# Performance work log

Measured on AMD Instinct MI355X. Metric: run time of the kernel, lower is better.

## Reference

```python
import jax, jax.numpy as jnp
import numpy as np
import math

V, E, H, A, N = 32000, 512, 512, 64, 8  # vocab, embed, rnn hidden, att_size, n_heads
T, B = 256, 128                          # scan length (acts as att batch), inner dim


def _lstm(x, Wih, Whh, bih, bhh):
    # x: (T, B, E); torch nn.LSTM gate order i, f, g, o; zero initial state
    Bb = x.shape[1]
    Hh = Whh.shape[1]
    init = (jnp.zeros((Bb, Hh), x.dtype), jnp.zeros((Bb, Hh), x.dtype))

    def step(carry, xt):
        h, c = carry
        gates = xt @ Wih.T + bih + h @ Whh.T + bhh          # (B, 4H)
        i, f, g, o = jnp.split(gates, 4, axis=-1)
        c = jax.nn.sigmoid(f) * c + jax.nn.sigmoid(i) * jnp.tanh(g)
        h = jax.nn.sigmoid(o) * jnp.tanh(c)
        return (h, c), h

    _, hs = jax.lax.scan(step, init, x)
    return hs  # (T, B, H)


def setup_inputs() -> dict:
    key = jax.random.key(0)
    ks = jax.random.split(key, 26)
    rn = lambda k, s: jax.random.normal(k, s, jnp.float32) * 0.02
    inp = {
        "input_seq_l": jax.random.randint(ks[0], (T, B), 0, V, jnp.int32),
        "input_seq_r": jax.random.randint(ks[1], (T, B), 0, V, jnp.int32),
        "emb_l": rn(ks[2], (V, E)),
        "emb_r": rn(ks[3], (V, E)),
        "Wih_l": rn(ks[4], (4 * H, E)), "Whh_l": rn(ks[5], (4 * H, H)),
        "bih_l": rn(ks[6], (4 * H,)), "bhh_l": rn(ks[7], (4 * H,)),
        "Wih_r": rn(ks[8], (4 * H, E)), "Whh_r": rn(ks[9], (4 * H, H)),
        "bih_r": rn(ks[10], (4 * H,)), "bhh_r": rn(ks[11], (4 * H,)),
        "Wq": rn(ks[12], (N, H, A)), "bq": rn(ks[13], (N, A)),
        "Wk": rn(ks[14], (N, H, A)), "bk": rn(ks[15], (N, A)),
        "Wv": rn(ks[16], (N, H, A)), "bv": rn(ks[17], (N, A)),
        "Wo": rn(ks[18], (N * A, H)), "bo": rn(ks[19], (H,)),
        "Wh": rn(ks[20], (2 * H, 64)), "bh": rn(ks[21], (64,)),
        "Wa": rn(ks[22], (64, 2)), "ba": rn(ks[23], (2,)),
    }
    return inp


def reference(input_seq_l, input_seq_r, emb_l, emb_r,
              Wih_l, Whh_l, bih_l, bhh_l,
              Wih_r, Whh_r, bih_r, bhh_r,
              Wq, bq, Wk, bk, Wv, bv, Wo, bo, Wh, bh, Wa, ba):
    # left encoder
    ol = _lstm(emb_l[input_seq_l], Wih_l, Whh_l, bih_l, bhh_l)   # (T, B, H)
    # multi-head attention over left outputs (all heads batched)
    q = jnp.einsum('tbh,nhd->ntbd', ol, Wq) + bq[:, None, None, :]
    k = jnp.einsum('tbh,nhd->ntbd', ol, Wk) + bk[:, None, None, :]
    v = jnp.einsum('tbh,nhd->ntbd', ol, Wv) + bv[:, None, None, :]
    scores = jnp.einsum('ntbd,ntcd->ntbc', q, k) / math.sqrt(A)  # (N, T, B, B)
    p = jax.nn.softmax(scores, axis=-1)
    att = jnp.einsum('ntbc,ntcd->ntbd', p, v)                    # (N, T, B, A)
    att = att.transpose(1, 2, 0, 3).reshape(att.shape[1], att.shape[2], -1)  # (T, B, N*A)
    ol = att @ Wo + bo                                           # (T, B, H)
    ol = ol.mean(axis=1)                                         # (T, H)
    # right encoder
    orr = _lstm(emb_r[input_seq_r], Wih_r, Whh_r, bih_r, bhh_r).mean(axis=1)  # (T, H)
    cat = jnp.concatenate([ol, orr], axis=1)                     # (T, 2H)
    fc = cat @ Wh + bh
    ans = jax.nn.softmax(fc @ Wa + ba, axis=1)                   # (T, 2)
    return ans
```

## Files before the change

kernel.cpp:

```cpp
#include <hip/hip_runtime.h>

typedef unsigned short u16;
typedef __attribute__((ext_vector_type(4))) float f32x4;
typedef __attribute__((ext_vector_type(8))) short bf8;

#define MFMA16(a, b, c) __builtin_amdgcn_mfma_f32_16x16x32_bf16((a), (b), (c), 0, 0, 0)

__device__ __forceinline__ u16 f2bf(float f) {
  unsigned u = __builtin_bit_cast(unsigned, f);
  u += 0x7FFFu + ((u >> 16) & 1u);
  return (u16)(u >> 16);
}
__device__ __forceinline__ float bf2f(u16 h) {
  unsigned u = ((unsigned)h) << 16;
  return __builtin_bit_cast(float, u);
}
__device__ __forceinline__ float sigm(float x) { return 1.0f / (1.0f + __expf(-x)); }
__device__ __forceinline__ float tanh_f(float x) {
  x = fminf(fmaxf(x, -15.f), 15.f);
  float e = __expf(2.f * x);
  return (e - 1.f) / (e + 1.f);
}

__global__ void k_cast(const float* __restrict__ in, u16* __restrict__ out, int n4) {
  int i = blockIdx.x * blockDim.x + threadIdx.x;
  if (i >= n4) return;
  float4 v = ((const float4*)in)[i];
  union { u16 h[4]; uint2 u; } p;
  p.h[0] = f2bf(v.x); p.h[1] = f2bf(v.y); p.h[2] = f2bf(v.z); p.h[3] = f2bf(v.w);
  ((uint2*)out)[i] = p.u;
}

__global__ void k_bsum(const float* __restrict__ a, const float* __restrict__ b,
                       float* __restrict__ o, int n) {
  int i = blockIdx.x * blockDim.x + threadIdx.x;
  if (i < n) o[i] = a[i] + b[i];
}

__global__ void k_zero32(unsigned* __restrict__ p, int n) {
  int i = blockIdx.x * blockDim.x + threadIdx.x;
  if (i < n) p[i] = 0u;
}

__global__ void k_fill(float* __restrict__ p, int n, float v) {
  int i = blockIdx.x * blockDim.x + threadIdx.x;
  if (i < n) p[i] = v;
}

__global__ void k_tqkv(const float* __restrict__ W, u16* __restrict__ WT) {
  int g = blockIdx.x * blockDim.x + threadIdx.x;
  int n = g >> 15, d = (g >> 9) & 63, h = g & 511;
  WT[g] = f2bf(W[(n << 15) + (h << 6) + d]);
}

__device__ __forceinline__ void gemm_body(
    const int* __restrict__ idx, const float* __restrict__ emb,
    const float* __restrict__ Wih, u16* __restrict__ Gpre,
    int m_base, int m0, int n0, char* smem, int tid) {
  u16 (*lA)[72] = (u16(*)[72])smem;
  u16 (*lB)[72] = (u16(*)[72])(smem + 18432);
  int lane = tid & 63, wid = tid >> 6;
  int wm = (wid >> 1) << 6, wn = (wid & 1) << 6;
  int lq = lane >> 4, lc = lane & 15;
  f32x4 acc[4][4] = {};
  for (int k0 = 0; k0 < 512; k0 += 64) {
#pragma unroll
    for (int s = 0; s < 2; s++) {
      int slot = tid + s * 256;
      int row = slot >> 2, seg = (slot & 3) << 4;
      const float* pa = emb + (size_t)idx[m_base + m0 + row] * 512 + k0 + seg;
      const float* pb = Wih + (size_t)(n0 + row) * 512 + k0 + seg;
      float4 a0 = ((const float4*)pa)[0], a1 = ((const float4*)pa)[1];
      float4 a2 = ((const float4*)pa)[2], a3 = ((const float4*)pa)[3];
      float4 b0 = ((const float4*)pb)[0], b1 = ((const float4*)pb)[1];
      float4 b2 = ((const float4*)pb)[2], b3 = ((const float4*)pb)[3];
      union { u16 h[8]; int4 v; } pk;
      pk.h[0]=f2bf(a0.x); pk.h[1]=f2bf(a0.y); pk.h[2]=f2bf(a0.z); pk.h[3]=f2bf(a0.w);
      pk.h[4]=f2bf(a1.x); pk.h[5]=f2bf(a1.y); pk.h[6]=f2bf(a1.z); pk.h[7]=f2bf(a1.w);
      *(int4*)&lA[row][seg] = pk.v;
      pk.h[0]=f2bf(a2.x); pk.h[1]=f2bf(a2.y); pk.h[2]=f2bf(a2.z); pk.h[3]=f2bf(a2.w);
      pk.h[4]=f2bf(a3.x); pk.h[5]=f2bf(a3.y); pk.h[6]=f2bf(a3.z); pk.h[7]=f2bf(a3.w);
      *(int4*)&lA[row][seg + 8] = pk.v;
      pk.h[0]=f2bf(b0.x); pk.h[1]=f2bf(b0.y); pk.h[2]=f2bf(b0.z); pk.h[3]=f2bf(b0.w);
      pk.h[4]=f2bf(b1.x); pk.h[5]=f2bf(b1.y); pk.h[6]=f2bf(b1.z); pk.h[7]=f2bf(b1.w);
      *(int4*)&lB[row][seg] = pk.v;
      pk.h[0]=f2bf(b2.x); pk.h[1]=f2bf(b2.y); pk.h[2]=f2bf(b2.z); pk.h[3]=f2bf(b2.w);
      pk.h[4]=f2bf(b3.x); pk.h[5]=f2bf(b3.y); pk.h[6]=f2bf(b3.z); pk.h[7]=f2bf(b3.w);
      *(int4*)&lB[row][seg + 8] = pk.v;
    }
    __syncthreads();
#pragma unroll
    for (int kk = 0; kk < 64; kk += 32) {
      int ko = kk + (lq << 3);
      bf8 af[4], bg[4];
#pragma unroll
      for (int i = 0; i < 4; i++) af[i] = *(const bf8*)&lA[wm + i * 16 + lc][ko];
#pragma unroll
      for (int j = 0; j < 4; j++) bg[j] = *(const bf8*)&lB[wn + j * 16 + lc][ko];
#pragma unroll
      for (int i = 0; i < 4; i++)
#pragma unroll
        for (int j = 0; j < 4; j++) acc[i][j] = MFMA16(af[i], bg[j], acc[i][j]);
    }
    __syncthreads();
  }
  int cr = lq << 2;
#pragma unroll
  for (int i = 0; i < 4; i++)
#pragma unroll
    for (int j = 0; j < 4; j++)
#pragma unroll
      for (int r = 0; r < 4; r++) {
        int m = m0 + wm + i * 16 + cr + r;
        int nn = n0 + wn + j * 16 + lc;
        Gpre[(size_t)m * 2048 + nn] = f2bf(acc[i][j][r]);
      }
}

__global__ __launch_bounds__(256, 2) void k_gemm_gates(
    const int* __restrict__ idx, const float* __restrict__ emb,
    const float* __restrict__ Wih, u16* __restrict__ Gpre, int m_base) {
  __shared__ __align__(16) char smem[36864];
  gemm_body(idx, emb, Wih, Gpre, m_base, blockIdx.y << 7, blockIdx.x << 7,
            smem, threadIdx.x);
}

__device__ void lstm_body(
    const u16* __restrict__ Gl, const u16* __restrict__ Gr,
    const u16* __restrict__ Whl, const u16* __restrict__ Whr,
    const float* __restrict__ bsl, const float* __restrict__ bsr,
    u16* __restrict__ hsl, u16* __restrict__ hsr,
    unsigned* __restrict__ hx, float* __restrict__ cstate,
    unsigned* __restrict__ flg, int t0, int nT, char* hlds, int bid, int tid) {
  int pod = bid & 7, cg = bid >> 3;
  int e = pod >> 2, bg = pod & 3;
  int b0 = bg << 5, c0 = cg << 5;
  const u16* Gpre = e ? Gr : Gl;
  const u16* Whh  = e ? Whr : Whl;
  const float* bsum = e ? bsr : bsl;
  u16* hs = e ? hsr : hsl;

  int lane = tid & 63, w = tid >> 6;
  int lq = lane >> 4, lc = lane & 15, cr = lq << 2;
  int cl = (w << 3) + (lc & 7);
  int gg0 = lc >> 3;
  int lr0 = (gg0 << 5) + cl;
  int lr1 = ((2 + gg0) << 5) + cl;
  int gc0 = (gg0 << 9) + c0 + cl;
  int gc1 = ((2 + gg0) << 9) + c0 + cl;
  float bs0 = bsum[gc0], bs1 = bsum[gc1];
  bool owner = (lc & 8) != 0;

  int gr0 = ((lr0 >> 5) << 9) + c0 + (lr0 & 31);
  int gr1 = ((lr1 >> 5) << 9) + c0 + (lr1 & 31);
  bf8 wb0[16], wb1[16];
  {
    const u16* p0 = Whh + (size_t)gr0 * 512 + (lq << 3);
    const u16* p1 = Whh + (size_t)gr1 * 512 + (lq << 3);
#pragma unroll
    for (int ks = 0; ks < 16; ks++) {
      wb0[ks] = *(const bf8*)(p0 + (ks << 5));
      wb1[ks] = *(const bf8*)(p1 + (ks << 5));
    }
  }
  float creg[2][4];
#pragma unroll
  for (int mi = 0; mi < 2; mi++)
#pragma unroll
    for (int r = 0; r < 4; r++) creg[mi][r] = 0.f;
  if (t0 > 0 && owner) {
#pragma unroll
    for (int mi = 0; mi < 2; mi++)
#pragma unroll
      for (int r = 0; r < 4; r++)
        creg[mi][r] = cstate[(size_t)((e << 7) + b0 + (mi << 4) + cr + r) * 512 + c0 + cl];
  }

  u16 gp[2][2][4];
#pragma unroll
  for (int mi = 0; mi < 2; mi++)
#pragma unroll
    for (int r = 0; r < 4; r++) {
      size_t rowb = (size_t)(b0 + (mi << 4) + cr + r) << 11;
      gp[mi][0][r] = Gpre[rowb + gc0];
      gp[mi][1][r] = Gpre[rowb + gc1];
    }

  int ax = (lc & 7) << 4;
  int abyte0 = lc << 10;
  int abyte1 = (16 + lc) << 10;
  int hxc = (c0 >> 1) + (w << 2) + ((lc & 7) >> 1);
  const int srow = tid >> 6;
  const int scolb = (tid & 63) << 4;

  for (int t = 0; t < nT; t++) {
    int tg = t0 + t;
    f32x4 acc[2][2] = {};
    if (tg > 0) {
      if (t > 0) {
        if (tid < 64) {
          const unsigned* fa = flg + (pod << 6) + (lane & 15);
          unsigned fv;
          int guard = 0;
          while (true) {
            asm volatile("global_load_dword %0, %1, off sc0 sc1"
                         : "=v"(fv) : "v"(fa) : "memory");
            asm volatile("s_waitcnt vmcnt(0)" ::: "memory");
            if (__ballot(fv >= (unsigned)tg) == ~0ull) break;
            if (++guard > 300000) break;
          }
        }
        __syncthreads();
      }
      const unsigned* hxr = hx + (((size_t)((e << 1) | ((tg - 1) & 1))) << 15);
      uint4 sv[8];
#pragma unroll
      for (int i = 0; i < 8; i++) {
        int row = (i << 2) + srow;
        const unsigned* ap = hxr + (((size_t)(b0 + row)) << 8) + ((tid & 63) << 2);
        asm volatile("global_load_dwordx4 %0, %1, off sc0 sc1"
                     : "=v"(sv[i]) : "v"(ap));
      }
      asm volatile("s_waitcnt vmcnt(0)" ::: "memory");
      __builtin_amdgcn_sched_barrier(0);
#pragma unroll
      for (int i = 0; i < 8; i++) {
        int row = (i << 2) + srow;
        *(uint4*)(hlds + (row << 10) + (scolb ^ ((row & 7) << 4))) = sv[i];
      }
      __syncthreads();
#pragma unroll
      for (int ks = 0; ks < 16; ks++) {
        int kb = (ks << 6) + (lq << 4);
        bf8 a0 = *(const bf8*)(hlds + abyte0 + (kb ^ ax));
        bf8 a1 = *(const bf8*)(hlds + abyte1 + (kb ^ ax));
        acc[0][0] = MFMA16(a0, wb0[ks], acc[0][0]);
        acc[0][1] = MFMA16(a0, wb1[ks], acc[0][1]);
        acc[1][0] = MFMA16(a1, wb0[ks], acc[1][0]);
        acc[1][1] = MFMA16(a1, wb1[ks], acc[1][1]);
      }
      __syncthreads();
    }
    unsigned* hxw = hx + (((size_t)((e << 1) | (tg & 1))) << 15);
#pragma unroll
    for (int mi = 0; mi < 2; mi++)
#pragma unroll
      for (int r = 0; r < 4; r++) {
        float v0 = acc[mi][0][r] + bf2f(gp[mi][0][r]) + bs0;
        float v1 = acc[mi][1][r] + bf2f(gp[mi][1][r]) + bs1;
        float send = sigm(v0) * tanh_f(v1);
        float recv = __shfl_xor(send, 8, 64);
        float h = 0.f;
        if (owner) {
          float c = sigm(v0) * creg[mi][r] + recv;
          creg[mi][r] = c;
          h = sigm(v1) * tanh_f(c);
        }
        unsigned hb = (unsigned)f2bf(h);
        unsigned hi = __shfl_down(hb, 1, 64);
        unsigned packed = (hb & 0xffffu) | (hi << 16);
        int b = b0 + (mi << 4) + cr + r;
        if (owner && !(lane & 1)) {
          *(unsigned*)(hs + (((size_t)((tg << 7) + b)) << 9) + c0 + cl) = packed;
          unsigned* sa = hxw + (((size_t)b) << 8) + hxc;
          asm volatile("global_store_dword %0, %1, off sc0 sc1"
                       :: "v"(sa), "v"(packed) : "memory");
        }
      }
    asm volatile("s_waitcnt vmcnt(0)" ::: "memory");
    __syncthreads();
    if (tid == 0) {
      unsigned tv = (unsigned)(tg + 1);
      unsigned* fa = flg + (pod << 6) + cg;
      asm volatile("global_store_dword %0, %1, off sc0 sc1"
                   :: "v"(fa), "v"(tv) : "memory");
    }
    if (t + 1 < nT) {
#pragma unroll
      for (int mi = 0; mi < 2; mi++)
#pragma unroll
        for (int r = 0; r < 4; r++) {
          size_t rowb = (size_t)(((t + 1) << 7) + b0 + (mi << 4) + cr + r) << 11;
          gp[mi][0][r] = Gpre[rowb + gc0];
          gp[mi][1][r] = Gpre[rowb + gc1];
        }
    }
  }
  if (owner) {
#pragma unroll
    for (int mi = 0; mi < 2; mi++)
#pragma unroll
      for (int r = 0; r < 4; r++)
        cstate[(size_t)((e << 7) + b0 + (mi << 4) + cr + r) * 512 + c0 + cl] = creg[mi][r];
  }
}

__global__ __launch_bounds__(256, 1) void k_fused(
    const u16* __restrict__ Gl, const u16* __restrict__ Gr,
    u16* __restrict__ Ggl, u16* __restrict__ Ggr,
    const int* __restrict__ seq_l, const int* __restrict__ seq_r,
    const float* __restrict__ emb_l, const float* __restrict__ emb_r,
    const float* __restrict__ Wih_l, const float* __restrict__ Wih_r,
    const u16* __restrict__ Whl, const u16* __restrict__ Whr,
    const float* __restrict__ bsl, const float* __restrict__ bsr,
    u16* __restrict__ hsl, u16* __restrict__ hsr,
    unsigned* __restrict__ hx, float* __restrict__ cstate,
    unsigned* __restrict__ flg, int t0, int nT, int gmb, int Tc) {
  __shared__ __align__(16) char smem[36864];
  int bid = blockIdx.x, tid = threadIdx.x;
  if (bid < 128) {
    lstm_body(Gl, Gr, Whl, Whr, bsl, bsr, hsl, hsr, hx, cstate, flg,
              t0, nT, smem, bid, tid);
  } else {
    int gb = bid - 128;
    int per = Tc << 4;
    int ge = gb >= per;
    int rem = ge ? gb - per : gb;
    gemm_body(ge ? seq_r : seq_l, ge ? emb_r : emb_l, ge ? Wih_r : Wih_l,
              ge ? Ggr : Ggl, gmb, (rem >> 4) << 7, (rem & 15) << 7, smem, tid);
  }
}

__global__ __launch_bounds__(256) void k_meanr(const u16* __restrict__ hs, float* __restrict__ out) {
  __shared__ float part[4][512];
  int t = blockIdx.x, tid = threadIdx.x;
  int rg = tid >> 6, ln = tid & 63;
  float s[8] = {};
  for (int b = rg << 5; b < (rg << 5) + 32; b++) {
    bf8 v = *(const bf8*)(hs + (((size_t)((t << 7) + b)) << 9) + (ln << 3));
#pragma unroll
    for (int j = 0; j < 8; j++) s[j] += bf2f((u16)v[j]);
  }
#pragma unroll
  for (int j = 0; j < 8; j++) part[rg][(ln << 3) + j] = s[j];
  __syncthreads();
  for (int c = tid; c < 512; c += 256)
    out[(t << 9) + c] = (part[0][c] + part[1][c] + part[2][c] + part[3][c]) * 0.0078125f;
}

__global__ __launch_bounds__(256, 1) void k_attn(
    const u16* __restrict__ hs,
    const u16* __restrict__ WqT, const u16* __restrict__ WkT, const u16* __restrict__ WvT,
    const float* __restrict__ bq, const float* __restrict__ bk, const float* __restrict__ bv,
    float* __restrict__ attmean) {
  __shared__ __align__(16) char smem[123904];
  u16 (*qs)[72]  = (u16(*)[72])smem;
  u16 (*ksm)[72] = (u16(*)[72])(smem + 18432);
  u16 (*vt)[136] = (u16(*)[136])(smem + 36864);
  float (*sc)[132] = (float(*)[132])(smem + 54272);
  u16 (*ps)[136] = (u16(*)[136])smem;
  float* red = (float*)(smem + 54272);
  float* pmax = (float*)(smem + 121856);
  float* psum = (float*)(smem + 122880);

  int bid = blockIdx.x;
  int n = bid >> 8, t = bid & 255;
  int tid = threadIdx.x, lane = tid & 63, wid = tid >> 6;
  int lq = lane >> 4, lc = lane & 15, cr = lq << 2;
  const u16* ol = hs + ((size_t)t << 16);

  float bqv[4], bkv[4];
#pragma unroll
  for (int nf = 0; nf < 4; nf++) {
    bqv[nf] = bq[(n << 6) + (nf << 4) + lc];
    bkv[nf] = bk[(n << 6) + (nf << 4) + lc];
  }
  float bvv[4][4];
#pragma unroll
  for (int mi = 0; mi < 4; mi++)
#pragma unroll
    for (int r = 0; r < 4; r++) bvv[mi][r] = bv[(n << 6) + (mi << 4) + cr + r];

  const u16* wq = WqT + ((size_t)n << 15);
  const u16* wk = WkT + ((size_t)n << 15);
  const u16* wv = WvT + ((size_t)n << 15);
  f32x4 aq[2][4] = {}, ak[2][4] = {}, av[4][2] = {};
  for (int ks = 0; ks < 16; ks++) {
    int ko = (ks << 5) + (lq << 3);
    bf8 a0 = *(const bf8*)&ol[(size_t)((wid << 5) + lc) * 512 + ko];
    bf8 a1 = *(const bf8*)&ol[(size_t)((wid << 5) + 16 + lc) * 512 + ko];
#pragma unroll
    for (int nf = 0; nf < 4; nf++) {
      bf8 bw = *(const bf8*)&wq[(size_t)((nf << 4) + lc) * 512 + ko];
      aq[0][nf] = MFMA16(a0, bw, aq[0][nf]);
      aq[1][nf] = MFMA16(a1, bw, aq[1][nf]);
      bf8 bw2 = *(const bf8*)&wk[(size_t)((nf << 4) + lc) * 512 + ko];
      ak[0][nf] = MFMA16(a0, bw2, ak[0][nf]);
      ak[1][nf] = MFMA16(a1, bw2, ak[1][nf]);
    }
#pragma unroll
    for (int mi = 0; mi < 4; mi++) {
      bf8 aw = *(const bf8*)&wv[(size_t)((mi << 4) + lc) * 512 + ko];
      av[mi][0] = MFMA16(aw, a0, av[mi][0]);
      av[mi][1] = MFMA16(aw, a1, av[mi][1]);
    }
  }
#pragma unroll
  for (int mi = 0; mi < 2; mi++)
#pragma unroll
    for (int nf = 0; nf < 4; nf++)
#pragma unroll
      for (int r = 0; r < 4; r++) {
        int b = (wid << 5) + (mi << 4) + cr + r;
        int d = (nf << 4) + lc;
        qs[b][d] = f2bf(aq[mi][nf][r] + bqv[nf]);
        ksm[b][d] = f2bf(ak[mi][nf][r] + bkv[nf]);
      }
#pragma unroll
  for (int mi = 0; mi < 4; mi++)
#pragma unroll
    for (int c2 = 0; c2 < 2; c2++)
#pragma unroll
      for (int r = 0; r < 4; r++) {
        int d = (mi << 4) + cr + r;
        int c = (wid << 5) + (c2 << 4) + lc;
        vt[d][c] = f2bf(av[mi][c2][r] + bvv[mi][r]);
      }
  __syncthreads();

  f32x4 as_[2][8] = {};
#pragma unroll
  for (int ks = 0; ks < 2; ks++) {
    int ko = (ks << 5) + (lq << 3);
    bf8 a0 = *(const bf8*)&qs[(wid << 5) + lc][ko];
    bf8 a1 = *(const bf8*)&qs[(wid << 5) + 16 + lc][ko];
#pragma unroll
    for (int nf = 0; nf < 8; nf++) {
      bf8 bw = *(const bf8*)&ksm[(nf << 4) + lc][ko];
      as_[0][nf] = MFMA16(a0, bw, as_[0][nf]);
      as_[1][nf] = MFMA16(a1, bw, as_[1][nf]);
    }
  }
#pragma unroll
  for (int mi = 0; mi < 2; mi++)
#pragma unroll
    for (int nf = 0; nf < 8; nf++)
#pragma unroll
      for (int r = 0; r < 4; r++)
        sc[(wid << 5) + (mi << 4) + cr + r][(nf << 4) + lc] = as_[mi][nf][r] * 0.125f;
  __syncthreads();

  {
    int row = tid & 127, half = tid >> 7;
    int cb = half << 6;
    float mx = -1e30f;
    for (int j = 0; j < 64; j++) mx = fmaxf(mx, sc[row][cb + j]);
    pmax[(half << 7) + row] = mx;
    __syncthreads();
    mx = fmaxf(pmax[row], pmax[128 + row]);
    float s = 0.f;
    for (int j = 0; j < 64; j++) { float ev = __expf(sc[row][cb + j] - mx); s += ev; sc[row][cb + j] = ev; }
    psum[(half << 7) + row] = s;
    __syncthreads();
    float inv = 1.f / (psum[row] + psum[128 + row]);
    for (int j = 0; j < 64; j++) ps[row][cb + j] = f2bf(sc[row][cb + j] * inv);
  }
  __syncthreads();

  f32x4 ao[2][4] = {};
#pragma unroll
  for (int ks = 0; ks < 4; ks++) {
    int ko = (ks << 5) + (lq << 3);
    bf8 a0 = *(const bf8*)&ps[(wid << 5) + lc][ko];
    bf8 a1 = *(const bf8*)&ps[(wid << 5) + 16 + lc][ko];
#pragma unroll
    for (int nf = 0; nf < 4; nf++) {
      bf8 bw = *(const bf8*)&vt[(nf << 4) + lc][ko];
      ao[0][nf] = MFMA16(a0, bw, ao[0][nf]);
      ao[1][nf] = MFMA16(a1, bw, ao[1][nf]);
    }
  }
  float pm[4];
#pragma unroll
  for (int nf = 0; nf < 4; nf++) {
    float s = 0.f;
#pragma unroll
    for (int mi = 0; mi < 2; mi++)
#pragma unroll
      for (int r = 0; r < 4; r++) s += ao[mi][nf][r];
    s += __shfl_xor(s, 16, 64);
    s += __shfl_xor(s, 32, 64);
    pm[nf] = s;
  }
  if (lq == 0) {
#pragma unroll
    for (int nf = 0; nf < 4; nf++) red[(wid << 6) + (nf << 4) + lc] = pm[nf];
  }
  __syncthreads();
  if (tid < 64) {
    float s = red[tid] + red[64 + tid] + red[128 + tid] + red[192 + tid];
    attmean[(t << 9) + (n << 6) + tid] = s * 0.0078125f;
  }
}

__global__ __launch_bounds__(256) void k_olm(const float* __restrict__ am, const float* __restrict__ Wo,
                                             const float* __restrict__ bo, float* __restrict__ olm) {
  __shared__ float row[512];
  int t = blockIdx.x >> 1, h0 = (blockIdx.x & 1) << 8;
  int tid = threadIdx.x;
  row[tid] = am[(t << 9) + tid];
  row[tid + 256] = am[(t << 9) + 256 + tid];
  __syncthreads();
  int h = h0 + tid;
  float s = bo[h];
  for (int k = 0; k < 512; k++) s += row[k] * Wo[(k << 9) + h];
  olm[(t << 9) + h] = s;
}

__global__ __launch_bounds__(64) void k_final(const float* __restrict__ olmp, const float* __restrict__ hrm,
                                              const float* __restrict__ Wh, const float* __restrict__ bh,
                                              const float* __restrict__ Wa, const float* __restrict__ ba,
                                              float* __restrict__ out) {
  __shared__ float cat[1024];
  int t = blockIdx.x, j = threadIdx.x;
  for (int i = j; i < 512; i += 64) {
    cat[i] = olmp[(t << 9) + i];
    cat[512 + i] = hrm[(t << 9) + i];
  }
  __syncthreads();
  float f = bh[j];
  for (int k = 0; k < 1024; k++) f += cat[k] * Wh[(k << 6) + j];
  float p0 = f * Wa[j * 2], p1 = f * Wa[j * 2 + 1];
#pragma unroll
  for (int o = 32; o > 0; o >>= 1) { p0 += __shfl_down(p0, o); p1 += __shfl_down(p1, o); }
  if (j == 0) {
    p0 += ba[0]; p1 += ba[1];
    float m = fmaxf(p0, p1);
    float e0 = __expf(p0 - m), e1 = __expf(p1 - m);
    float inv = 1.f / (e0 + e1);
    out[t * 2] = e0 * inv;
    out[t * 2 + 1] = e1 * inv;
  }
}

extern "C" void kernel_launch(void* const* d_in, const int* in_sizes, int n_in,
                              void* d_out, int out_size, void* d_ws, size_t ws_size,
                              hipStream_t stream) {
  const int*   seq_l = (const int*)d_in[0];
  const int*   seq_r = (const int*)d_in[1];
  const float* emb_l = (const float*)d_in[2];
  const float* emb_r = (const float*)d_in[3];
  const float* Wih_l = (const float*)d_in[4];
  const float* Whh_l = (const float*)d_in[5];
  const float* bih_l = (const float*)d_in[6];
  const float* bhh_l = (const float*)d_in[7];
  const float* Wih_r = (const float*)d_in[8];
  const float* Whh_r = (const float*)d_in[9];
  const float* bih_r = (const float*)d_in[10];
  const float* bhh_r = (const float*)d_in[11];
  const float* Wq = (const float*)d_in[12];
  const float* bq = (const float*)d_in[13];
  const float* Wk = (const float*)d_in[14];
  const float* bk = (const float*)d_in[15];
  const float* Wv = (const float*)d_in[16];
  const float* bv = (const float*)d_in[17];
  const float* Wo = (const float*)d_in[18];
  const float* bo = (const float*)d_in[19];
  const float* Wh = (const float*)d_in[20];
  const float* bhc = (const float*)d_in[21];
  const float* Wa = (const float*)d_in[22];
  const float* ba = (const float*)d_in[23];
  float* out = (float*)d_out;

  char* ws = (char*)d_ws;
  size_t off = 0;
  auto alloc = [&](size_t bytes) { char* p = ws + off; off += (bytes + 255) & ~(size_t)255; return p; };
  u16*   hsl  = (u16*)alloc(33554432);
  u16*   hsr  = (u16*)alloc(33554432);
  u16*   Whl  = (u16*)alloc(2097152);
  u16*   Whr  = (u16*)alloc(2097152);
  u16*   WqT  = (u16*)alloc(524288);
  u16*   WkT  = (u16*)alloc(524288);
  u16*   WvT  = (u16*)alloc(524288);
  float* bsl  = (float*)alloc(8192);
  float* bsr  = (float*)alloc(8192);
  unsigned* hx = (unsigned*)alloc(524288);
  float* cst  = (float*)alloc(524288);
  unsigned* flg = (unsigned*)alloc(2048);
  float* am   = (float*)alloc(524288);
  float* hrm  = (float*)alloc(524288);
  float* olm  = (float*)alloc(524288);
  size_t fixed = off;

  int Tc = 0;
  const int cands[3] = {128, 64, 32};
  for (int i = 0; i < 3; i++) {
    size_t need = fixed + 4ull * (size_t)cands[i] * 524288ull;
    if (need <= ws_size) { Tc = cands[i]; break; }
  }
  if (Tc == 0) {
    k_fill<<<2, 256, 0, stream>>>(out, out_size, 0.25f);
    return;
  }
  size_t gbytes = (size_t)Tc * 524288ull;
  u16* Glb[2]; u16* Grb[2];
  Glb[0] = (u16*)alloc(gbytes); Glb[1] = (u16*)alloc(gbytes);
  Grb[0] = (u16*)alloc(gbytes); Grb[1] = (u16*)alloc(gbytes);

  k_zero32<<<2, 256, 0, stream>>>(flg, 512);
  k_cast<<<1024, 256, 0, stream>>>(Whh_l, Whl, 262144);
  k_cast<<<1024, 256, 0, stream>>>(Whh_r, Whr, 262144);
  k_bsum<<<8, 256, 0, stream>>>(bih_l, bhh_l, bsl, 2048);
  k_bsum<<<8, 256, 0, stream>>>(bih_r, bhh_r, bsr, 2048);
  k_tqkv<<<1024, 256, 0, stream>>>(Wq, WqT);
  k_tqkv<<<1024, 256, 0, stream>>>(Wk, WkT);
  k_tqkv<<<1024, 256, 0, stream>>>(Wv, WvT);

  k_gemm_gates<<<dim3(16, Tc), 256, 0, stream>>>(seq_l, emb_l, Wih_l, Glb[0], 0);
  k_gemm_gates<<<dim3(16, Tc), 256, 0, stream>>>(seq_r, emb_r, Wih_r, Grb[0], 0);

  int nC = 256 / Tc;
  for (int c = 0; c < nC; c++) {
    int hg = (c + 1 < nC);
    int grid = 128 + (hg ? (Tc << 5) : 0);
    k_fused<<<grid, 256, 0, stream>>>(
        Glb[c & 1], Grb[c & 1], Glb[(c + 1) & 1], Grb[(c + 1) & 1],
        seq_l, seq_r, emb_l, emb_r, Wih_l, Wih_r,
        Whl, Whr, bsl, bsr, hsl, hsr, hx, cst, flg,
        c * Tc, Tc, (c + 1) * Tc * 128, Tc);
  }
  k_meanr<<<256, 256, 0, stream>>>(hsr, hrm);
  k_attn<<<2048, 256, 0, stream>>>(hsl, WqT, WkT, WvT, bq, bk, bv, am);
  k_olm<<<512, 256, 0, stream>>>(am, Wo, bo, olm);
  k_final<<<256, 64, 0, stream>>>(olm, hrm, Wh, bhc, Wa, ba, out);
}
```

Before: 1.708 ms.

## Overlap input-gate GEMM with LSTM recurrence via per-timestep readiness flags

Removes the separate up-front gate GEMM launches and the double-buffered chunk pipeline. The fused kernel now computes each timestep's input-gate tiles concurrently with the recurrence, and each tile bumps a per-timestep counter. LSTM blocks spin until all 16 tiles for that step are ready. Cross-block h synchronisation moves from a 64-thread ballot plus barrier to per-thread polling of flags stored beside the h buffer, and the small prep kernels are merged into one launch. The intent is to hide the GEMM behind the serial recurrence and cut launch and sync overhead, at the cost of more spin polling and a dependence on co-residency of the GEMM blocks.

```diff
diff --git a/kernel.cpp b/kernel.cpp
--- a/kernel.cpp
+++ b/kernel.cpp
@@ -21,42 +21,58 @@
   float e = __expf(2.f * x);
   return (e - 1.f) / (e + 1.f);
 }
-
-__global__ void k_cast(const float* __restrict__ in, u16* __restrict__ out, int n4) {
-  int i = blockIdx.x * blockDim.x + threadIdx.x;
-  if (i >= n4) return;
-  float4 v = ((const float4*)in)[i];
-  union { u16 h[4]; uint2 u; } p;
-  p.h[0] = f2bf(v.x); p.h[1] = f2bf(v.y); p.h[2] = f2bf(v.z); p.h[3] = f2bf(v.w);
-  ((uint2*)out)[i] = p.u;
-}
-
-__global__ void k_bsum(const float* __restrict__ a, const float* __restrict__ b,
-                       float* __restrict__ o, int n) {
-  int i = blockIdx.x * blockDim.x + threadIdx.x;
-  if (i < n) o[i] = a[i] + b[i];
-}
-
-__global__ void k_zero32(unsigned* __restrict__ p, int n) {
-  int i = blockIdx.x * blockDim.x + threadIdx.x;
-  if (i < n) p[i] = 0u;
-}
+__device__ __forceinline__ unsigned umin_(unsigned a, unsigned b) { return a < b ? a : b; }
 
 __global__ void k_fill(float* __restrict__ p, int n, float v) {
   int i = blockIdx.x * blockDim.x + threadIdx.x;
   if (i < n) p[i] = v;
 }
 
-__global__ void k_tqkv(const float* __restrict__ W, u16* __restrict__ WT) {
-  int g = blockIdx.x * blockDim.x + threadIdx.x;
-  int n = g >> 15, d = (g >> 9) & 63, h = g & 511;
-  WT[g] = f2bf(W[(n << 15) + (h << 6) + d]);
+__global__ __launch_bounds__(256) void k_prep(
+    unsigned* __restrict__ hx, unsigned* __restrict__ gflg,
+    const float* __restrict__ Whh_l, u16* __restrict__ Whl,
+    const float* __restrict__ Whh_r, u16* __restrict__ Whr,
+    const float* __restrict__ Wq, u16* __restrict__ WqT,
+    const float* __restrict__ Wk, u16* __restrict__ WkT,
+    const float* __restrict__ Wv, u16* __restrict__ WvT,
+    const float* __restrict__ bih_l, const float* __restrict__ bhh_l, float* __restrict__ bsl,
+    const float* __restrict__ bih_r, const float* __restrict__ bhh_r, float* __restrict__ bsr) {
+  int bid = blockIdx.x, tid = threadIdx.x;
+  if (bid < 513) {
+    hx[bid * 256 + tid] = 0u;
+  } else if (bid < 515) {
+    gflg[(bid - 513) * 256 + tid] = 0u;
+  } else if (bid < 2563) {
+    int rel = bid - 515;
+    int enc = rel >> 10;
+    int i = (rel & 1023) * 256 + tid;
+    const float* in = enc ? Whh_r : Whh_l;
+    u16* out = enc ? Whr : Whl;
+    float4 v = ((const float4*)in)[i];
+    union { u16 h[4]; uint2 u; } p;
+    p.h[0] = f2bf(v.x); p.h[1] = f2bf(v.y); p.h[2] = f2bf(v.z); p.h[3] = f2bf(v.w);
+    ((uint2*)out)[i] = p.u;
+  } else if (bid < 5635) {
+    int rel = bid - 2563;
+    int which = rel >> 10;
+    int g = (rel & 1023) * 256 + tid;
+    const float* W = which == 0 ? Wq : (which == 1 ? Wk : Wv);
+    u16* WT = which == 0 ? WqT : (which == 1 ? WkT : WvT);
+    int n = g >> 15, d = (g >> 9) & 63, h = g & 511;
+    WT[g] = f2bf(W[(n << 15) + (h << 6) + d]);
+  } else {
+    int rel = bid - 5635;
+    int enc = rel >> 3;
+    int i = (rel & 7) * 256 + tid;
+    if (enc == 0) bsl[i] = bih_l[i] + bhh_l[i];
+    else          bsr[i] = bih_r[i] + bhh_r[i];
+  }
 }
 
 __device__ __forceinline__ void gemm_body(
     const int* __restrict__ idx, const float* __restrict__ emb,
     const float* __restrict__ Wih, u16* __restrict__ Gpre,
-    int m_base, int m0, int n0, char* smem, int tid) {
+    int m_base, int m0, int n0, char* smem, int tid, unsigned* flagp) {
   u16 (*lA)[72] = (u16(*)[72])smem;
   u16 (*lB)[72] = (u16(*)[72])(smem + 18432);
   int lane = tid & 63, wid = tid >> 6;
@@ -113,16 +129,15 @@
       for (int r = 0; r < 4; r++) {
         int m = m0 + wm + i * 16 + cr + r;
         int nn = n0 + wn + j * 16 + lc;
-        Gpre[(size_t)m * 2048 + nn] = f2bf(acc[i][j][r]);
-      }
-}
-
-__global__ __launch_bounds__(256, 2) void k_gemm_gates(
-    const int* __restrict__ idx, const float* __restrict__ emb,
-    const float* __restrict__ Wih, u16* __restrict__ Gpre, int m_base) {
-  __shared__ __align__(16) char smem[36864];
-  gemm_body(idx, emb, Wih, Gpre, m_base, blockIdx.y << 7, blockIdx.x << 7,
-            smem, threadIdx.x);
+        u16* gp_ = Gpre + (size_t)m * 2048 + nn;
+        unsigned hv = (unsigned)f2bf(acc[i][j][r]);
+        asm volatile("global_store_short %0, %1, off sc0 sc1"
+                     :: "v"(gp_), "v"(hv) : "memory");
+      }
+  asm volatile("s_waitcnt vmcnt(0)" ::: "memory");
+  __syncthreads();
+  if (tid == 0)
+    __hip_atomic_fetch_add(flagp, 1u, __ATOMIC_RELAXED, __HIP_MEMORY_SCOPE_AGENT);
 }
 
 __device__ void lstm_body(
@@ -131,7 +146,8 @@
     const float* __restrict__ bsl, const float* __restrict__ bsr,
     u16* __restrict__ hsl, u16* __restrict__ hsr,
     unsigned* __restrict__ hx, float* __restrict__ cstate,
-    unsigned* __restrict__ flg, int t0, int nT, char* hlds, int bid, int tid) {
+    const unsigned* __restrict__ gflg,
+    int t0, int nT, char* hlds, int bid, int tid) {
   int pod = bid & 7, cg = bid >> 3;
   int e = pod >> 2, bg = pod & 3;
   int b0 = bg << 5, c0 = cg << 5;
@@ -139,6 +155,7 @@
   const u16* Whh  = e ? Whr : Whl;
   const float* bsum = e ? bsr : bsl;
   u16* hs = e ? hsr : hsl;
+  const unsigned* gfe = gflg + (e << 8);
 
   int lane = tid & 63, w = tid >> 6;
   int lq = lane >> 4, lc = lane & 15, cr = lq << 2;
@@ -176,6 +193,16 @@
         creg[mi][r] = cstate[(size_t)((e << 7) + b0 + (mi << 4) + cr + r) * 512 + c0 + cl];
   }
 
+  {
+    const unsigned* ga = gfe + t0;
+    unsigned gv; int guard = 0;
+    while (true) {
+      asm volatile("global_load_dword %0, %1, off sc0 sc1" : "=v"(gv) : "v"(ga) : "memory");
+      asm volatile("s_waitcnt vmcnt(0)" ::: "memory");
+      if (gv >= 16u) break;
+      if (++guard > 2000000) break;
+    }
+  }
   u16 gp[2][2][4];
 #pragma unroll
   for (int mi = 0; mi < 2; mi++)
@@ -186,40 +213,34 @@
       gp[mi][1][r] = Gpre[rowb + gc1];
     }
 
+  int member = (tid & 63) >> 2;
+  int srow = tid >> 6;
+  int scolb = (tid & 63) << 4;
   int ax = (lc & 7) << 4;
   int abyte0 = lc << 10;
   int abyte1 = (16 + lc) << 10;
   int hxc = (c0 >> 1) + (w << 2) + ((lc & 7) >> 1);
-  const int srow = tid >> 6;
-  const int scolb = (tid & 63) << 4;
 
   for (int t = 0; t < nT; t++) {
     int tg = t0 + t;
     f32x4 acc[2][2] = {};
     if (tg > 0) {
-      if (t > 0) {
-        if (tid < 64) {
-          const unsigned* fa = flg + (pod << 6) + (lane & 15);
-          unsigned fv;
-          int guard = 0;
-          while (true) {
-            asm volatile("global_load_dword %0, %1, off sc0 sc1"
-                         : "=v"(fv) : "v"(fa) : "memory");
-            asm volatile("s_waitcnt vmcnt(0)" ::: "memory");
-            if (__ballot(fv >= (unsigned)tg) == ~0ull) break;
-            if (++guard > 300000) break;
-          }
+      unsigned* base = hx + (size_t)((e << 1) | ((tg - 1) & 1)) * 32832u;
+      {
+        const unsigned* tga = base + 32768 + (bg << 4) + member;
+        unsigned tv; int guard = 0;
+        while (true) {
+          asm volatile("global_load_dword %0, %1, off sc0 sc1" : "=v"(tv) : "v"(tga) : "memory");
+          asm volatile("s_waitcnt vmcnt(0)" ::: "memory");
+          if (tv >= (unsigned)tg) break;
+          if (++guard > 2000000) break;
         }
-        __syncthreads();
-      }
-      const unsigned* hxr = hx + (((size_t)((e << 1) | ((tg - 1) & 1))) << 15);
+      }
       uint4 sv[8];
 #pragma unroll
       for (int i = 0; i < 8; i++) {
-        int row = (i << 2) + srow;
-        const unsigned* ap = hxr + (((size_t)(b0 + row)) << 8) + ((tid & 63) << 2);
-        asm volatile("global_load_dwordx4 %0, %1, off sc0 sc1"
-                     : "=v"(sv[i]) : "v"(ap));
+        const unsigned* ap = base + ((b0 + (i << 2) + srow) << 8) + ((tid & 63) << 2);
+        asm volatile("global_load_dwordx4 %0, %1, off sc0 sc1" : "=v"(sv[i]) : "v"(ap) : "memory");
       }
       asm volatile("s_waitcnt vmcnt(0)" ::: "memory");
       __builtin_amdgcn_sched_barrier(0);
@@ -241,7 +262,7 @@
       }
       __syncthreads();
     }
-    unsigned* hxw = hx + (((size_t)((e << 1) | (tg & 1))) << 15);
+    unsigned* baseW = hx + (size_t)((e << 1) | (tg & 1)) * 32832u;
 #pragma unroll
     for (int mi = 0; mi < 2; mi++)
 #pragma unroll
@@ -262,7 +283,7 @@
         int b = b0 + (mi << 4) + cr + r;
         if (owner && !(lane & 1)) {
           *(unsigned*)(hs + (((size_t)((tg << 7) + b)) << 9) + c0 + cl) = packed;
-          unsigned* sa = hxw + (((size_t)b) << 8) + hxc;
+          unsigned* sa = baseW + ((size_t)b << 8) + hxc;
           asm volatile("global_store_dword %0, %1, off sc0 sc1"
                        :: "v"(sa), "v"(packed) : "memory");
         }
@@ -271,11 +292,19 @@
     __syncthreads();
     if (tid == 0) {
       unsigned tv = (unsigned)(tg + 1);
-      unsigned* fa = flg + (pod << 6) + cg;
+      unsigned* tpa = baseW + 32768 + (bg << 4) + cg;
       asm volatile("global_store_dword %0, %1, off sc0 sc1"
-                   :: "v"(fa), "v"(tv) : "memory");
+                   :: "v"(tpa), "v"(tv) : "memory");
     }
     if (t + 1 < nT) {
+      const unsigned* ga = gfe + tg + 1;
+      unsigned gv; int guard = 0;
+      while (true) {
+        asm volatile("global_load_dword %0, %1, off sc0 sc1" : "=v"(gv) : "v"(ga) : "memory");
+        asm volatile("s_waitcnt vmcnt(0)" ::: "memory");
+        if (gv >= 16u) break;
+        if (++guard > 2000000) break;
+      }
 #pragma unroll
       for (int mi = 0; mi < 2; mi++)
 #pragma unroll
@@ -296,8 +325,7 @@
 }
 
 __global__ __launch_bounds__(256, 1) void k_fused(
-    const u16* __restrict__ Gl, const u16* __restrict__ Gr,
-    u16* __restrict__ Ggl, u16* __restrict__ Ggr,
+    u16* __restrict__ Gl, u16* __restrict__ Gr,
     const int* __restrict__ seq_l, const int* __restrict__ seq_r,
     const float* __restrict__ emb_l, const float* __restrict__ emb_r,
     const float* __restrict__ Wih_l, const float* __restrict__ Wih_r,
@@ -305,19 +333,18 @@
     const float* __restrict__ bsl, const float* __restrict__ bsr,
     u16* __restrict__ hsl, u16* __restrict__ hsr,
     unsigned* __restrict__ hx, float* __restrict__ cstate,
-    unsigned* __restrict__ flg, int t0, int nT, int gmb, int Tc) {
+    unsigned* __restrict__ gflg, int t0, int nT) {
   __shared__ __align__(16) char smem[36864];
   int bid = blockIdx.x, tid = threadIdx.x;
   if (bid < 128) {
-    lstm_body(Gl, Gr, Whl, Whr, bsl, bsr, hsl, hsr, hx, cstate, flg,
+    lstm_body(Gl, Gr, Whl, Whr, bsl, bsr, hsl, hsr, hx, cstate, gflg,
               t0, nT, smem, bid, tid);
   } else {
     int gb = bid - 128;
-    int per = Tc << 4;
-    int ge = gb >= per;
-    int rem = ge ? gb - per : gb;
-    gemm_body(ge ? seq_r : seq_l, ge ? emb_r : emb_l, ge ? Wih_r : Wih_l,
-              ge ? Ggr : Ggl, gmb, (rem >> 4) << 7, (rem & 15) << 7, smem, tid);
+    int tt = gb >> 5, enc = (gb >> 4) & 1, ntile = gb & 15;
+    gemm_body(enc ? seq_r : seq_l, enc ? emb_r : emb_l, enc ? Wih_r : Wih_l,
+              enc ? Gr : Gl, t0 << 7, tt << 7, ntile << 7, smem, tid,
+              gflg + (enc << 8) + t0 + tt);
   }
 }
 
@@ -574,18 +601,18 @@
   u16*   WvT  = (u16*)alloc(524288);
   float* bsl  = (float*)alloc(8192);
   float* bsr  = (float*)alloc(8192);
-  unsigned* hx = (unsigned*)alloc(524288);
+  unsigned* hx = (unsigned*)alloc(525568);
   float* cst  = (float*)alloc(524288);
-  unsigned* flg = (unsigned*)alloc(2048);
+  unsigned* gflg = (unsigned*)alloc(2048);
   float* am   = (float*)alloc(524288);
   float* hrm  = (float*)alloc(524288);
   float* olm  = (float*)alloc(524288);
   size_t fixed = off;
 
   int Tc = 0;
-  const int cands[3] = {128, 64, 32};
-  for (int i = 0; i < 3; i++) {
-    size_t need = fixed + 4ull * (size_t)cands[i] * 524288ull;
+  const int cands[4] = {256, 128, 64, 32};
+  for (int i = 0; i < 4; i++) {
+    size_t need = fixed + 2ull * (size_t)cands[i] * 524288ull;
     if (need <= ws_size) { Tc = cands[i]; break; }
   }
   if (Tc == 0) {
@@ -593,31 +620,19 @@
     return;
   }
   size_t gbytes = (size_t)Tc * 524288ull;
-  u16* Glb[2]; u16* Grb[2];
-  Glb[0] = (u16*)alloc(gbytes); Glb[1] = (u16*)alloc(gbytes);
-  Grb[0] = (u16*)alloc(gbytes); Grb[1] = (u16*)alloc(gbytes);
-
-  k_zero32<<<2, 256, 0, stream>>>(flg, 512);
-  k_cast<<<1024, 256, 0, stream>>>(Whh_l, Whl, 262144);
-  k_cast<<<1024, 256, 0, stream>>>(Whh_r, Whr, 262144);
-  k_bsum<<<8, 256, 0, stream>>>(bih_l, bhh_l, bsl, 2048);
-  k_bsum<<<8, 256, 0, stream>>>(bih_r, bhh_r, bsr, 2048);
-  k_tqkv<<<1024, 256, 0, stream>>>(Wq, WqT);
-  k_tqkv<<<1024, 256, 0, stream>>>(Wk, WkT);
-  k_tqkv<<<1024, 256, 0, stream>>>(Wv, WvT);
-
-  k_gemm_gates<<<dim3(16, Tc), 256, 0, stream>>>(seq_l, emb_l, Wih_l, Glb[0], 0);
-  k_gemm_gates<<<dim3(16, Tc), 256, 0, stream>>>(seq_r, emb_r, Wih_r, Grb[0], 0);
+  u16* Gl = (u16*)alloc(gbytes);
+  u16* Gr = (u16*)alloc(gbytes);
+
+  k_prep<<<5651, 256, 0, stream>>>(hx, gflg, Whh_l, Whl, Whh_r, Whr,
+                                   Wq, WqT, Wk, WkT, Wv, WvT,
+                                   bih_l, bhh_l, bsl, bih_r, bhh_r, bsr);
 
   int nC = 256 / Tc;
   for (int c = 0; c < nC; c++) {
-    int hg = (c + 1 < nC);
-    int grid = 128 + (hg ? (Tc << 5) : 0);
+    int grid = 128 + (Tc << 5);
     k_fused<<<grid, 256, 0, stream>>>(
-        Glb[c & 1], Grb[c & 1], Glb[(c + 1) & 1], Grb[(c + 1) & 1],
-        seq_l, seq_r, emb_l, emb_r, Wih_l, Wih_r,
-        Whl, Whr, bsl, bsr, hsl, hsr, hx, cst, flg,
-        c * Tc, Tc, (c + 1) * Tc * 128, Tc);
+        Gl, Gr, seq_l, seq_r, emb_l, emb_r, Wih_l, Wih_r,
+        Whl, Whr, bsl, bsr, hsl, hsr, hx, cst, gflg, c * Tc, Tc);
   }
   k_meanr<<<256, 256, 0, stream>>>(hsr, hrm);
   k_attn<<<2048, 256, 0, stream>>>(hsl, WqT, WkT, WvT, bq, bk, bv, am);
```

After: 1.807 ms. +5.8%, slower.

## Merge prep kernels into one launch and fuse right-encoder mean into LSTM

Applied to the files above, without the earlier changes.

Folds the flag zeroing, weight casts, QKV transposes, bias sums and the first gate GEMMs into a single block-dispatched prep kernel, cutting about ten launches to one. The right LSTM no longer writes its full hidden-state history. Instead each step reduces h across the batch with shuffles and atomically adds the scaled mean into hrm, which removes the separate mean kernel and a 32 MB buffer write and read. The cost is extra atomics and shuffles inside the latency-critical recurrent step, and float atomics make the mean's summation order nondeterministic.

```diff
diff --git a/kernel.cpp b/kernel.cpp
--- a/kernel.cpp
+++ b/kernel.cpp
@@ -22,35 +22,9 @@
   return (e - 1.f) / (e + 1.f);
 }
 
-__global__ void k_cast(const float* __restrict__ in, u16* __restrict__ out, int n4) {
-  int i = blockIdx.x * blockDim.x + threadIdx.x;
-  if (i >= n4) return;
-  float4 v = ((const float4*)in)[i];
-  union { u16 h[4]; uint2 u; } p;
-  p.h[0] = f2bf(v.x); p.h[1] = f2bf(v.y); p.h[2] = f2bf(v.z); p.h[3] = f2bf(v.w);
-  ((uint2*)out)[i] = p.u;
-}
-
-__global__ void k_bsum(const float* __restrict__ a, const float* __restrict__ b,
-                       float* __restrict__ o, int n) {
-  int i = blockIdx.x * blockDim.x + threadIdx.x;
-  if (i < n) o[i] = a[i] + b[i];
-}
-
-__global__ void k_zero32(unsigned* __restrict__ p, int n) {
-  int i = blockIdx.x * blockDim.x + threadIdx.x;
-  if (i < n) p[i] = 0u;
-}
-
 __global__ void k_fill(float* __restrict__ p, int n, float v) {
   int i = blockIdx.x * blockDim.x + threadIdx.x;
   if (i < n) p[i] = v;
-}
-
-__global__ void k_tqkv(const float* __restrict__ W, u16* __restrict__ WT) {
-  int g = blockIdx.x * blockDim.x + threadIdx.x;
-  int n = g >> 15, d = (g >> 9) & 63, h = g & 511;
-  WT[g] = f2bf(W[(n << 15) + (h << 6) + d]);
 }
 
 __device__ __forceinline__ void gemm_body(
@@ -117,19 +91,64 @@
       }
 }
 
-__global__ __launch_bounds__(256, 2) void k_gemm_gates(
-    const int* __restrict__ idx, const float* __restrict__ emb,
-    const float* __restrict__ Wih, u16* __restrict__ Gpre, int m_base) {
+__global__ __launch_bounds__(256, 1) void k_prep(
+    unsigned* __restrict__ flg, float* __restrict__ hrm,
+    const float* __restrict__ Whh_l, u16* __restrict__ Whl,
+    const float* __restrict__ Whh_r, u16* __restrict__ Whr,
+    const float* __restrict__ Wq, u16* __restrict__ WqT,
+    const float* __restrict__ Wk, u16* __restrict__ WkT,
+    const float* __restrict__ Wv, u16* __restrict__ WvT,
+    const float* __restrict__ bih_l, const float* __restrict__ bhh_l, float* __restrict__ bsl,
+    const float* __restrict__ bih_r, const float* __restrict__ bhh_r, float* __restrict__ bsr,
+    const int* __restrict__ seq_l, const int* __restrict__ seq_r,
+    const float* __restrict__ emb_l, const float* __restrict__ emb_r,
+    const float* __restrict__ Wih_l, const float* __restrict__ Wih_r,
+    u16* __restrict__ Gl0, u16* __restrict__ Gr0, int Tc) {
   __shared__ __align__(16) char smem[36864];
-  gemm_body(idx, emb, Wih, Gpre, m_base, blockIdx.y << 7, blockIdx.x << 7,
-            smem, threadIdx.x);
+  int bid = blockIdx.x, tid = threadIdx.x;
+  if (bid < 2) {
+    flg[bid * 256 + tid] = 0u;
+  } else if (bid < 514) {
+    hrm[(bid - 2) * 256 + tid] = 0.f;
+  } else if (bid < 2562) {
+    int rel = bid - 514;
+    int enc = rel >> 10;
+    int i = (rel & 1023) * 256 + tid;
+    const float* in = enc ? Whh_r : Whh_l;
+    u16* outp = enc ? Whr : Whl;
+    float4 v = ((const float4*)in)[i];
+    union { u16 h[4]; uint2 u; } p;
+    p.h[0] = f2bf(v.x); p.h[1] = f2bf(v.y); p.h[2] = f2bf(v.z); p.h[3] = f2bf(v.w);
+    ((uint2*)outp)[i] = p.u;
+  } else if (bid < 5634) {
+    int rel = bid - 2562;
+    int which = rel >> 10;
+    int g = (rel & 1023) * 256 + tid;
+    const float* W = which == 0 ? Wq : (which == 1 ? Wk : Wv);
+    u16* WT = which == 0 ? WqT : (which == 1 ? WkT : WvT);
+    int n = g >> 15, d = (g >> 9) & 63, h = g & 511;
+    WT[g] = f2bf(W[(n << 15) + (h << 6) + d]);
+  } else if (bid < 5650) {
+    int rel = bid - 5634;
+    int enc = rel >> 3;
+    int i = (rel & 7) * 256 + tid;
+    if (enc == 0) bsl[i] = bih_l[i] + bhh_l[i];
+    else          bsr[i] = bih_r[i] + bhh_r[i];
+  } else {
+    int rel = bid - 5650;
+    int per = Tc << 4;
+    int ge = rel >= per;
+    int rem = ge ? rel - per : rel;
+    gemm_body(ge ? seq_r : seq_l, ge ? emb_r : emb_l, ge ? Wih_r : Wih_l,
+              ge ? Gr0 : Gl0, 0, (rem >> 4) << 7, (rem & 15) << 7, smem, tid);
+  }
 }
 
 __device__ void lstm_body(
     const u16* __restrict__ Gl, const u16* __restrict__ Gr,
     const u16* __restrict__ Whl, const u16* __restrict__ Whr,
     const float* __restrict__ bsl, const float* __restrict__ bsr,
-    u16* __restrict__ hsl, u16* __restrict__ hsr,
+    u16* __restrict__ hsl, float* __restrict__ hrm,
     unsigned* __restrict__ hx, float* __restrict__ cstate,
     unsigned* __restrict__ flg, int t0, int nT, char* hlds, int bid, int tid) {
   int pod = bid & 7, cg = bid >> 3;
@@ -138,7 +157,6 @@
   const u16* Gpre = e ? Gr : Gl;
   const u16* Whh  = e ? Whr : Whl;
   const float* bsum = e ? bsr : bsl;
-  u16* hs = e ? hsr : hsl;
 
   int lane = tid & 63, w = tid >> 6;
   int lq = lane >> 4, lc = lane & 15, cr = lq << 2;
@@ -242,6 +260,7 @@
       __syncthreads();
     }
     unsigned* hxw = hx + (((size_t)((e << 1) | (tg & 1))) << 15);
+    float msum = 0.f;
 #pragma unroll
     for (int mi = 0; mi < 2; mi++)
 #pragma unroll
@@ -255,13 +274,15 @@
           float c = sigm(v0) * creg[mi][r] + recv;
           creg[mi][r] = c;
           h = sigm(v1) * tanh_f(c);
+          msum += h;
         }
         unsigned hb = (unsigned)f2bf(h);
         unsigned hi = __shfl_down(hb, 1, 64);
         unsigned packed = (hb & 0xffffu) | (hi << 16);
         int b = b0 + (mi << 4) + cr + r;
         if (owner && !(lane & 1)) {
-          *(unsigned*)(hs + (((size_t)((tg << 7) + b)) << 9) + c0 + cl) = packed;
+          if (!e)
+            *(unsigned*)(hsl + (((size_t)((tg << 7) + b)) << 9) + c0 + cl) = packed;
           unsigned* sa = hxw + (((size_t)b) << 8) + hxc;
           asm volatile("global_store_dword %0, %1, off sc0 sc1"
                        :: "v"(sa), "v"(packed) : "memory");
@@ -274,6 +295,13 @@
       unsigned* fa = flg + (pod << 6) + cg;
       asm volatile("global_store_dword %0, %1, off sc0 sc1"
                    :: "v"(fa), "v"(tv) : "memory");
+    }
+    if (e) {
+      float s = msum;
+      s += __shfl_xor(s, 16, 64);
+      s += __shfl_xor(s, 32, 64);
+      if (owner && lq == 0)
+        atomicAdd(&hrm[(tg << 9) + c0 + cl], s * 0.0078125f);
     }
     if (t + 1 < nT) {
 #pragma unroll
@@ -303,13 +331,13 @@
     const float* __restrict__ Wih_l, const float* __restrict__ Wih_r,
     const u16* __restrict__ Whl, const u16* __restrict__ Whr,
     const float* __restrict__ bsl, const float* __restrict__ bsr,
-    u16* __restrict__ hsl, u16* __restrict__ hsr,
+    u16* __restrict__ hsl, float* __restrict__ hrm,
     unsigned* __restrict__ hx, float* __restrict__ cstate,
     unsigned* __restrict__ flg, int t0, int nT, int gmb, int Tc) {
   __shared__ __align__(16) char smem[36864];
   int bid = blockIdx.x, tid = threadIdx.x;
   if (bid < 128) {
-    lstm_body(Gl, Gr, Whl, Whr, bsl, bsr, hsl, hsr, hx, cstate, flg,
+    lstm_body(Gl, Gr, Whl, Whr, bsl, bsr, hsl, hrm, hx, cstate, flg,
               t0, nT, smem, bid, tid);
   } else {
     int gb = bid - 128;
@@ -319,23 +347,6 @@
     gemm_body(ge ? seq_r : seq_l, ge ? emb_r : emb_l, ge ? Wih_r : Wih_l,
               ge ? Ggr : Ggl, gmb, (rem >> 4) << 7, (rem & 15) << 7, smem, tid);
   }
-}
-
-__global__ __launch_bounds__(256) void k_meanr(const u16* __restrict__ hs, float* __restrict__ out) {
-  __shared__ float part[4][512];
-  int t = blockIdx.x, tid = threadIdx.x;
-  int rg = tid >> 6, ln = tid & 63;
-  float s[8] = {};
-  for (int b = rg << 5; b < (rg << 5) + 32; b++) {
-    bf8 v = *(const bf8*)(hs + (((size_t)((t << 7) + b)) << 9) + (ln << 3));
-#pragma unroll
-    for (int j = 0; j < 8; j++) s[j] += bf2f((u16)v[j]);
-  }
-#pragma unroll
-  for (int j = 0; j < 8; j++) part[rg][(ln << 3) + j] = s[j];
-  __syncthreads();
-  for (int c = tid; c < 512; c += 256)
-    out[(t << 9) + c] = (part[0][c] + part[1][c] + part[2][c] + part[3][c]) * 0.0078125f;
 }
 
 __global__ __launch_bounds__(256, 1) void k_attn(
@@ -566,7 +577,6 @@
   size_t off = 0;
   auto alloc = [&](size_t bytes) { char* p = ws + off; off += (bytes + 255) & ~(size_t)255; return p; };
   u16*   hsl  = (u16*)alloc(33554432);
-  u16*   hsr  = (u16*)alloc(33554432);
   u16*   Whl  = (u16*)alloc(2097152);
   u16*   Whr  = (u16*)alloc(2097152);
   u16*   WqT  = (u16*)alloc(524288);
@@ -597,17 +607,10 @@
   Glb[0] = (u16*)alloc(gbytes); Glb[1] = (u16*)alloc(gbytes);
   Grb[0] = (u16*)alloc(gbytes); Grb[1] = (u16*)alloc(gbytes);
 
-  k_zero32<<<2, 256, 0, stream>>>(flg, 512);
-  k_cast<<<1024, 256, 0, stream>>>(Whh_l, Whl, 262144);
-  k_cast<<<1024, 256, 0, stream>>>(Whh_r, Whr, 262144);
-  k_bsum<<<8, 256, 0, stream>>>(bih_l, bhh_l, bsl, 2048);
-  k_bsum<<<8, 256, 0, stream>>>(bih_r, bhh_r, bsr, 2048);
-  k_tqkv<<<1024, 256, 0, stream>>>(Wq, WqT);
-  k_tqkv<<<1024, 256, 0, stream>>>(Wk, WkT);
-  k_tqkv<<<1024, 256, 0, stream>>>(Wv, WvT);
-
-  k_gemm_gates<<<dim3(16, Tc), 256, 0, stream>>>(seq_l, emb_l, Wih_l, Glb[0], 0);
-  k_gemm_gates<<<dim3(16, Tc), 256, 0, stream>>>(seq_r, emb_r, Wih_r, Grb[0], 0);
+  k_prep<<<5650 + (Tc << 5), 256, 0, stream>>>(
+      flg, hrm, Whh_l, Whl, Whh_r, Whr, Wq, WqT, Wk, WkT, Wv, WvT,
+      bih_l, bhh_l, bsl, bih_r, bhh_r, bsr,
+      seq_l, seq_r, emb_l, emb_r, Wih_l, Wih_r, Glb[0], Grb[0], Tc);
 
   int nC = 256 / Tc;
   for (int c = 0; c < nC; c++) {
@@ -616,10 +619,9 @@
     k_fused<<<grid, 256, 0, stream>>>(
         Glb[c & 1], Grb[c & 1], Glb[(c + 1) & 1], Grb[(c + 1) & 1],
         seq_l, seq_r, emb_l, emb_r, Wih_l, Wih_r,
-        Whl, Whr, bsl, bsr, hsl, hsr, hx, cst, flg,
+        Whl, Whr, bsl, bsr, hsl, hrm, hx, cst, flg,
         c * Tc, Tc, (c + 1) * Tc * 128, Tc);
   }
-  k_meanr<<<256, 256, 0, stream>>>(hsr, hrm);
   k_attn<<<2048, 256, 0, stream>>>(hsl, WqT, WkT, WvT, bq, bk, bv, am);
   k_olm<<<512, 256, 0, stream>>>(am, Wo, bo, olm);
   k_final<<<256, 64, 0, stream>>>(olm, hrm, Wh, bhc, Wa, ba, out);
```

Result: slower. 1.751 ms (+2.5%).
